# Optimization experiments

Measured on AMD Instinct MI355X. Metric: run time of the kernel, lower is better.

## Reference

```python
import jax, jax.numpy as jnp
import numpy as np

N = 20000
IN_CH = 256
HID = 32
HEADS = 8
OUT_CH = 40
NEG_SLOPE = 0.2


def _gat_layer(x, src, dst, W, a_src, a_dst, b, heads, ch, concat):
    # x: [N, F_in], W: [F_in, heads*ch], a_src/a_dst: [heads, ch], b: [heads*ch] or [ch]
    n = x.shape[0]
    h = (x @ W).reshape(n, heads, ch)                      # [N, H, C]
    alpha_s = jnp.einsum('nhc,hc->nh', h, a_src)           # [N, H]
    alpha_d = jnp.einsum('nhc,hc->nh', h, a_dst)           # [N, H]
    e = jax.nn.leaky_relu(alpha_s[src] + alpha_d[dst], NEG_SLOPE)  # [E, H]
    # segment softmax over edges sharing the same destination node
    m = jax.ops.segment_max(e, dst, num_segments=n)        # [N, H]
    ex = jnp.exp(e - m[dst])                               # [E, H]
    denom = jax.ops.segment_sum(ex, dst, num_segments=n)   # [N, H]
    alpha = ex / (denom[dst] + 1e-16)                      # [E, H]
    out = jax.ops.segment_sum(h[src] * alpha[:, :, None], dst, num_segments=n)  # [N, H, C]
    out = out.reshape(n, heads * ch) if concat else out.mean(axis=1)
    return out + b


def setup_inputs() -> dict:
    key = jax.random.key(0)
    ks = jax.random.split(key, 12)
    x = jax.random.normal(ks[0], (N, IN_CH), dtype=jnp.float32)
    edge_index = jax.random.randint(ks[1], (2, 320000), 0, N, dtype=jnp.int64)
    s1 = 1.0 / np.sqrt(IN_CH)
    s2 = 1.0 / np.sqrt(HEADS * HID)
    W1 = jax.random.uniform(ks[2], (IN_CH, HEADS * HID), jnp.float32, -s1, s1)
    a1_src = jax.random.uniform(ks[3], (HEADS, HID), jnp.float32, -s2, s2)
    a1_dst = jax.random.uniform(ks[4], (HEADS, HID), jnp.float32, -s2, s2)
    b1 = jnp.zeros((HEADS * HID,), jnp.float32)
    W2 = jax.random.uniform(ks[5], (HEADS * HID, OUT_CH), jnp.float32, -s2, s2)
    so = 1.0 / np.sqrt(OUT_CH)
    a2_src = jax.random.uniform(ks[6], (1, OUT_CH), jnp.float32, -so, so)
    a2_dst = jax.random.uniform(ks[7], (1, OUT_CH), jnp.float32, -so, so)
    b2 = jnp.zeros((OUT_CH,), jnp.float32)
    return {"x": x, "edge_index": edge_index, "W1": W1, "a1_src": a1_src,
            "a1_dst": a1_dst, "b1": b1, "W2": W2, "a2_src": a2_src,
            "a2_dst": a2_dst, "b2": b2}


def reference(x, edge_index, W1, a1_src, a1_dst, b1, W2, a2_src, a2_dst, b2):
    n = x.shape[0]
    loop = jnp.arange(n, dtype=edge_index.dtype)
    src = jnp.concatenate([edge_index[0], loop])  # PyG adds self-loops by default
    dst = jnp.concatenate([edge_index[1], loop])
    # dropout layers are identity in eval mode
    h = _gat_layer(x, src, dst, W1, a1_src, a1_dst, b1, HEADS, HID, concat=True)
    h = jax.nn.elu(h)
    out = _gat_layer(h, src, dst, W2, a2_src, a2_dst, b2, 1, OUT_CH, concat=False)
    return jax.nn.log_softmax(out, axis=1)
```

## Files before the change

kernel.cpp:

```cpp
#include <hip/hip_runtime.h>
#include <math.h>

#define N_NODES 20000
#define E_RAW   320000
#define E_TOT   (E_RAW + N_NODES)
#define IN_CH   256
#define HEADS   8
#define HID     32
#define HH      (HEADS*HID)
#define OUT_CH  40
#define NC2     48
#define NEG     0.2f

#define HIST_BLKS ((E_TOT + 255) / 256)
#define G1_BLKS   313

typedef __attribute__((ext_vector_type(8))) short  short8;
typedef __attribute__((ext_vector_type(4))) float  floatx4;

__device__ __forceinline__ unsigned short f2bf(float f) {
    unsigned int u = __float_as_uint(f);
    unsigned int r = (u + 0x7FFFu + ((u >> 16) & 1u)) >> 16;
    return (unsigned short)r;
}
__device__ __forceinline__ float bf2f(unsigned short h) {
    return __uint_as_float(((unsigned int)h) << 16);
}
__device__ __forceinline__ float lexp(float v) {
    v = (v > 0.f) ? v : NEG * v;
    return __expf(v);
}


__global__ void setup_hist(const int* __restrict__ ei,
                           const float* __restrict__ W1,
                           const float* __restrict__ W2,
                           unsigned short* __restrict__ w1t,
                           unsigned short* __restrict__ w2t,
                           int* __restrict__ deg,
                           int* __restrict__ pos) {
    int b = blockIdx.x;
    int t = threadIdx.x;
    if (b < HIST_BLKS) {
        int e = b * 256 + t;
        if (e >= E_TOT) return;
        int d = (e < E_RAW) ? ei[E_RAW + e] : (e - E_RAW);
        pos[e] = atomicAdd(&deg[d], 1);
    } else if (b < HIST_BLKS + HH) {
        int c = b - HIST_BLKS;
        w1t[c * IN_CH + t] = f2bf(W1[(size_t)t * HH + c]);
    } else {
        int c = b - HIST_BLKS - HH;
        w2t[c * HH + t] = (c < OUT_CH) ? f2bf(W2[(size_t)t * OUT_CH + c]) : (unsigned short)0;
    }
}


__global__ __launch_bounds__(1024) void scan_kernel(const int* __restrict__ deg,
                                                    int* __restrict__ offs) {
    __shared__ int wsum[16], wpre[16];
    int t = threadIdx.x;
    int lane = t & 63, wave = t >> 6;
    const int chunk = 20;
    int begin = t * chunk;
    bool in = (begin < N_NODES);
    int loc[20];
    if (in) {
        #pragma unroll
        for (int v4 = 0; v4 < 5; v4++) {
            int4 v = *reinterpret_cast<const int4*>(&deg[begin + v4 * 4]);
            loc[v4*4+0] = v.x; loc[v4*4+1] = v.y; loc[v4*4+2] = v.z; loc[v4*4+3] = v.w;
        }
    } else {
        #pragma unroll
        for (int i = 0; i < 20; i++) loc[i] = 0;
    }
    int s = 0;
    #pragma unroll
    for (int i = 0; i < 20; i++) s += loc[i];
    int sc = s;
    #pragma unroll
    for (int off = 1; off < 64; off <<= 1) {
        int v = __shfl_up(sc, off);
        if (lane >= off) sc += v;
    }
    if (lane == 63) wsum[wave] = sc;
    __syncthreads();
    if (t < 16) {
        int v = wsum[t];
        int p = v;
        #pragma unroll
        for (int off = 1; off < 16; off <<= 1) {
            int u = __shfl_up(p, off);
            if (t >= off) p += u;
        }
        wpre[t] = p - v;
    }
    __syncthreads();
    int run = wpre[wave] + sc - s;
    if (in) {
        #pragma unroll
        for (int v4 = 0; v4 < 5; v4++) {
            int4 o;
            o.x = run; run += loc[v4*4+0];
            o.y = run; run += loc[v4*4+1];
            o.z = run; run += loc[v4*4+2];
            o.w = run; run += loc[v4*4+3];
            *reinterpret_cast<int4*>(&offs[begin + v4 * 4]) = o;
        }
    }
    if (t == 0) offs[N_NODES] = E_TOT;
}

#define G1_LDK 72
__global__ __launch_bounds__(256) void gemm1(const float* __restrict__ x,
                                             const unsigned short* __restrict__ w1t,
                                             const float* __restrict__ a1s,
                                             const float* __restrict__ a1d,
                                             unsigned short* __restrict__ h1b,
                                             float* __restrict__ as1,
                                             float* __restrict__ ad1,
                                             const int* __restrict__ ei,
                                             const int* __restrict__ offs,
                                             const int* __restrict__ pos,
                                             int* __restrict__ csr) {
    __shared__ unsigned short As[64 * G1_LDK];
    __shared__ unsigned short Bs[256 * G1_LDK];
    int t = threadIdx.x;

    if (blockIdx.x >= G1_BLKS) {
        int e = (blockIdx.x - G1_BLKS) * 256 + t;
        if (e < E_TOT) {
            int s, d;
            if (e < E_RAW) { s = ei[e]; d = ei[E_RAW + e]; }
            else           { s = e - E_RAW; d = s; }
            csr[offs[d] + pos[e]] = s;
        }
        return;
    }

    int wave = t >> 6, lane = t & 63;
    int ln = lane & 15, q = lane >> 4;
    int n0 = blockIdx.x * 64;

    floatx4 acc[16];
    #pragma unroll
    for (int f = 0; f < 16; f++) acc[f] = (floatx4){0.f, 0.f, 0.f, 0.f};

    int srow = t >> 4, scol = t & 15;

    for (int kc = 0; kc < IN_CH; kc += 64) {
        #pragma unroll
        for (int pp = 0; pp < 4; pp++) {
            int row = srow + pp * 16;
            int n = n0 + row;
            float4 v = (n < N_NODES)
                ? *reinterpret_cast<const float4*>(&x[(size_t)n * IN_CH + kc + scol * 4])
                : make_float4(0.f, 0.f, 0.f, 0.f);
            ushort4 pv;
            pv.x = f2bf(v.x); pv.y = f2bf(v.y); pv.z = f2bf(v.z); pv.w = f2bf(v.w);
            *reinterpret_cast<ushort4*>(&As[row * G1_LDK + scol * 4]) = pv;
        }
        #pragma unroll
        for (int pp = 0; pp < 16; pp++) {
            int row = srow + pp * 16;
            *reinterpret_cast<ushort4*>(&Bs[row * G1_LDK + scol * 4]) =
                *reinterpret_cast<const ushort4*>(&w1t[(size_t)row * IN_CH + kc + scol * 4]);
        }
        __syncthreads();
        #pragma unroll
        for (int ks = 0; ks < 2; ks++) {
            short8 a = *reinterpret_cast<const short8*>(
                &As[(16 * wave + ln) * G1_LDK + ks * 32 + q * 8]);
            #pragma unroll
            for (int f = 0; f < 16; f++) {
                short8 b = *reinterpret_cast<const short8*>(
                    &Bs[(16 * f + ln) * G1_LDK + ks * 32 + q * 8]);
                acc[f] = __builtin_amdgcn_mfma_f32_16x16x32_bf16(a, b, acc[f], 0, 0, 0);
            }
        }
        __syncthreads();
    }

    float Asr[16], Adr[16];
    #pragma unroll
    for (int f = 0; f < 16; f++) {
        Asr[f] = a1s[16 * f + ln];
        Adr[f] = a1d[16 * f + ln];
    }
    #pragma unroll
    for (int f = 0; f < 16; f++) {
        #pragma unroll
        for (int r = 0; r < 4; r++) {
            int n = n0 + 16 * wave + q * 4 + r;
            if (n < N_NODES)
                h1b[(size_t)n * HH + 16 * f + ln] = f2bf(acc[f][r]);
        }
    }
    #pragma unroll
    for (int lh = 0; lh < 8; lh++) {
        #pragma unroll
        for (int r = 0; r < 4; r++) {
            float ps = acc[2*lh][r] * Asr[2*lh] + acc[2*lh+1][r] * Asr[2*lh+1];
            float pd = acc[2*lh][r] * Adr[2*lh] + acc[2*lh+1][r] * Adr[2*lh+1];
            ps += __shfl_xor(ps, 1); ps += __shfl_xor(ps, 2);
            ps += __shfl_xor(ps, 4); ps += __shfl_xor(ps, 8);
            pd += __shfl_xor(pd, 1); pd += __shfl_xor(pd, 2);
            pd += __shfl_xor(pd, 4); pd += __shfl_xor(pd, 8);
            int n = n0 + 16 * wave + q * 4 + r;
            if (ln == 0 && n < N_NODES) {
                as1[n * HEADS + lh] = ps;
                ad1[n * HEADS + lh] = pd;
            }
        }
    }
}


__global__ __launch_bounds__(256) void aggr1(const unsigned short* __restrict__ h1b,
                                             const float* __restrict__ as1,
                                             const float* __restrict__ ad1,
                                             const float* __restrict__ b1,
                                             const int* __restrict__ offs,
                                             const int* __restrict__ csr,
                                             unsigned short* __restrict__ h2b) {
    int d = blockIdx.x * 4 + (threadIdx.x >> 6);
    int lane = threadIdx.x & 63;
    int h = lane >> 3;
    int c4 = lane * 4;
    int start = offs[d];
    int deg = offs[d + 1] - start;
    float adv = ad1[d * HEADS + h];

    float a0 = 0.f, a1 = 0.f, a2 = 0.f, a3 = 0.f, den = 0.f;
    int jj = 0;
    for (; jj + 8 <= deg; jj += 8) {
        int s[8];
        #pragma unroll
        for (int i = 0; i < 8; i++) s[i] = csr[start + jj + i];
        float e[8];
        #pragma unroll
        for (int i = 0; i < 8; i++) e[i] = as1[s[i] * HEADS + h];
        ushort4 pv[8];
        #pragma unroll
        for (int i = 0; i < 8; i++)
            pv[i] = *reinterpret_cast<const ushort4*>(&h1b[(size_t)s[i] * HH + c4]);
        #pragma unroll
        for (int i = 0; i < 8; i++) {
            float w = lexp(e[i] + adv);
            den += w;
            a0 = fmaf(bf2f(pv[i].x), w, a0);
            a1 = fmaf(bf2f(pv[i].y), w, a1);
            a2 = fmaf(bf2f(pv[i].z), w, a2);
            a3 = fmaf(bf2f(pv[i].w), w, a3);
        }
    }
    for (; jj < deg; jj++) {
        int s = csr[start + jj];
        float w = lexp(as1[s * HEADS + h] + adv);
        den += w;
        ushort4 pv = *reinterpret_cast<const ushort4*>(&h1b[(size_t)s * HH + c4]);
        a0 = fmaf(bf2f(pv.x), w, a0);
        a1 = fmaf(bf2f(pv.y), w, a1);
        a2 = fmaf(bf2f(pv.z), w, a2);
        a3 = fmaf(bf2f(pv.w), w, a3);
    }
    float inv = 1.0f / (den + 1e-16f);
    float4 bv = *reinterpret_cast<const float4*>(&b1[c4]);
    float r0 = a0 * inv + bv.x;
    float r1 = a1 * inv + bv.y;
    float r2 = a2 * inv + bv.z;
    float r3 = a3 * inv + bv.w;
    r0 = (r0 > 0.f) ? r0 : (__expf(r0) - 1.f);
    r1 = (r1 > 0.f) ? r1 : (__expf(r1) - 1.f);
    r2 = (r2 > 0.f) ? r2 : (__expf(r2) - 1.f);
    r3 = (r3 > 0.f) ? r3 : (__expf(r3) - 1.f);
    ushort4 ov;
    ov.x = f2bf(r0); ov.y = f2bf(r1); ov.z = f2bf(r2); ov.w = f2bf(r3);
    *reinterpret_cast<ushort4*>(&h2b[(size_t)d * HH + c4]) = ov;
}

#define G2_LDK 264
__global__ __launch_bounds__(256) void gemm2(const unsigned short* __restrict__ h2b,
                                             const unsigned short* __restrict__ w2t,
                                             const float* __restrict__ a2s,
                                             const float* __restrict__ a2d,
                                             unsigned short* __restrict__ h3b,
                                             float* __restrict__ as2,
                                             float* __restrict__ ad2) {
    __shared__ unsigned short As2[64 * G2_LDK];
    __shared__ unsigned short Bs2[NC2 * G2_LDK];
    int t = threadIdx.x;
    int wave = t >> 6, lane = t & 63;
    int ln = lane & 15, q = lane >> 4;
    int n0 = blockIdx.x * 64;

    {
        int row = t >> 2, seg = t & 3;
        int n = n0 + row;
        #pragma unroll
        for (int i = 0; i < 8; i++) {
            short8 v;
            if (n < N_NODES)
                v = *reinterpret_cast<const short8*>(&h2b[(size_t)n * HH + seg * 64 + i * 8]);
            else
                v = (short8){0,0,0,0,0,0,0,0};
            *reinterpret_cast<short8*>(&As2[row * G2_LDK + seg * 64 + i * 8]) = v;
        }
    }
    for (int u = t; u < NC2 * 32; u += 256) {
        int row = u >> 5;
        int col = (u & 31) * 8;
        *reinterpret_cast<short8*>(&Bs2[row * G2_LDK + col]) =
            *reinterpret_cast<const short8*>(&w2t[(size_t)row * HH + col]);
    }
    __syncthreads();

    floatx4 acc[3];
    #pragma unroll
    for (int f = 0; f < 3; f++) acc[f] = (floatx4){0.f, 0.f, 0.f, 0.f};

    #pragma unroll
    for (int kf = 0; kf < 8; kf++) {
        short8 a = *reinterpret_cast<const short8*>(
            &As2[(16 * wave + ln) * G2_LDK + kf * 32 + q * 8]);
        #pragma unroll
        for (int f = 0; f < 3; f++) {
            short8 b = *reinterpret_cast<const short8*>(
                &Bs2[(16 * f + ln) * G2_LDK + kf * 32 + q * 8]);
            acc[f] = __builtin_amdgcn_mfma_f32_16x16x32_bf16(a, b, acc[f], 0, 0, 0);
        }
    }

    float a2sv[3], a2dv[3];
    #pragma unroll
    for (int f = 0; f < 3; f++) {
        int c = 16 * f + ln;
        a2sv[f] = (c < OUT_CH) ? a2s[c] : 0.f;
        a2dv[f] = (c < OUT_CH) ? a2d[c] : 0.f;
    }
    #pragma unroll
    for (int r = 0; r < 4; r++) {
        int n = n0 + 16 * wave + q * 4 + r;
        float ps = acc[0][r] * a2sv[0] + acc[1][r] * a2sv[1] + acc[2][r] * a2sv[2];
        float pd = acc[0][r] * a2dv[0] + acc[1][r] * a2dv[1] + acc[2][r] * a2dv[2];
        ps += __shfl_xor(ps, 1); ps += __shfl_xor(ps, 2);
        ps += __shfl_xor(ps, 4); ps += __shfl_xor(ps, 8);
        pd += __shfl_xor(pd, 1); pd += __shfl_xor(pd, 2);
        pd += __shfl_xor(pd, 4); pd += __shfl_xor(pd, 8);
        if (n < N_NODES) {
            #pragma unroll
            for (int f = 0; f < 3; f++) {
                int c = 16 * f + ln;
                if (c < OUT_CH)
                    h3b[(size_t)n * OUT_CH + c] = f2bf(acc[f][r]);
            }
            if (ln == 0) { as2[n] = ps; ad2[n] = pd; }
        }
    }
}


__global__ __launch_bounds__(256) void aggr2(const unsigned short* __restrict__ h3b,
                                             const float* __restrict__ as2,
                                             const float* __restrict__ ad2,
                                             const float* __restrict__ b2,
                                             const int* __restrict__ offs,
                                             const int* __restrict__ csr,
                                             float* __restrict__ out) {
    int d = blockIdx.x * 4 + (threadIdx.x >> 6);
    int lane = threadIdx.x & 63;
    int start = offs[d];
    int deg = offs[d + 1] - start;
    float adv = ad2[d];
    bool ok = (lane < OUT_CH);
    int cl = ok ? lane : 0;

    float acc = 0.f, den = 0.f;
    int jj = 0;
    for (; jj + 8 <= deg; jj += 8) {
        int s[8];
        #pragma unroll
        for (int i = 0; i < 8; i++) s[i] = csr[start + jj + i];
        float e[8];
        #pragma unroll
        for (int i = 0; i < 8; i++) e[i] = as2[s[i]];
        unsigned short qv[8];
        #pragma unroll
        for (int i = 0; i < 8; i++) qv[i] = h3b[(size_t)s[i] * OUT_CH + cl];
        #pragma unroll
        for (int i = 0; i < 8; i++) {
            float w = lexp(e[i] + adv);
            den += w;
            acc = fmaf(bf2f(qv[i]), w, acc);
        }
    }
    for (; jj < deg; jj++) {
        int s = csr[start + jj];
        float w = lexp(as2[s] + adv);
        den += w;
        acc = fmaf(bf2f(h3b[(size_t)s * OUT_CH + cl]), w, acc);
    }

    float r = ok ? (acc / (den + 1e-16f) + b2[lane]) : -1e30f;
    float mx = r;
    #pragma unroll
    for (int off = 32; off >= 1; off >>= 1) mx = fmaxf(mx, __shfl_xor(mx, off));
    float ex = ok ? __expf(r - mx) : 0.f;
    float se = ex;
    #pragma unroll
    for (int off = 32; off >= 1; off >>= 1) se += __shfl_xor(se, off);
    if (ok) out[(size_t)d * OUT_CH + lane] = r - mx - __logf(se);
}


extern "C" void kernel_launch(void* const* d_in, const int* in_sizes, int n_in,
                              void* d_out, int out_size, void* d_ws, size_t ws_size,
                              hipStream_t stream) {
    const float* x   = (const float*)d_in[0];
    const int*   ei  = (const int*)  d_in[1];
    const float* W1  = (const float*)d_in[2];
    const float* a1s = (const float*)d_in[3];
    const float* a1d = (const float*)d_in[4];
    const float* b1  = (const float*)d_in[5];
    const float* W2  = (const float*)d_in[6];
    const float* a2s = (const float*)d_in[7];
    const float* a2d = (const float*)d_in[8];
    const float* b2  = (const float*)d_in[9];
    float* out = (float*)d_out;

    char* p = (char*)d_ws;
    auto alloc = [&](size_t bytes) {
        char* r = p;
        p += (bytes + 255) & ~(size_t)255;
        return r;
    };
    unsigned short* h1b = (unsigned short*)alloc((size_t)N_NODES * HH * 2);
    unsigned short* h2b = (unsigned short*)alloc((size_t)N_NODES * HH * 2);
    unsigned short* h3b = (unsigned short*)alloc((size_t)N_NODES * OUT_CH * 2);
    unsigned short* w1t = (unsigned short*)alloc((size_t)IN_CH * HH * 2);
    unsigned short* w2t = (unsigned short*)alloc((size_t)NC2 * HH * 2);
    float* as1  = (float*)alloc((size_t)N_NODES * HEADS * 4);
    float* ad1  = (float*)alloc((size_t)N_NODES * HEADS * 4);
    float* as2v = (float*)alloc((size_t)N_NODES * 4);
    float* ad2v = (float*)alloc((size_t)N_NODES * 4);
    int* deg    = (int*)alloc((size_t)N_NODES * 4);
    int* pos    = (int*)alloc((size_t)E_TOT * 4);
    int* offs   = (int*)alloc((size_t)(N_NODES + 1) * 4);
    int* csr    = (int*)alloc((size_t)E_TOT * 4);

    hipMemsetAsync(deg, 0, (size_t)N_NODES * sizeof(int), stream);
    setup_hist<<<HIST_BLKS + HH + NC2, 256, 0, stream>>>(ei, W1, W2, w1t, w2t, deg, pos);
    scan_kernel<<<1, 1024, 0, stream>>>(deg, offs);
    gemm1<<<G1_BLKS + HIST_BLKS, 256, 0, stream>>>(x, w1t, a1s, a1d, h1b, as1, ad1,
                                                   ei, offs, pos, csr);
    aggr1<<<N_NODES / 4, 256, 0, stream>>>(h1b, as1, ad1, b1, offs, csr, h2b);
    gemm2<<<313, 256, 0, stream>>>(h2b, w2t, a2s, a2d, h3b, as2v, ad2v);
    aggr2<<<N_NODES / 4, 256, 0, stream>>>(h3b, as2v, ad2v, b2, offs, csr, out);
}
```

Measured before the change: 192.7 us.

## Pre-convert x to bf16 and stage GEMM tiles via direct global-to-LDS loads

x is converted to bf16 once in the setup kernel. Both GEMMs now fill shared memory with global_load_lds 16-byte direct copies into XOR-swizzled tiles, replacing register-staged padded loads. gemm1 keeps the whole 64x256 A tile resident and streams B in K chunks. This is meant to cut VGPR staging and LDS bank conflicts, but it adds an extra bf16 copy of x in the workspace, extra setup blocks, and unguarded reads past N_NODES that depend on padded buffers. The padding rows are never initialized, though they only feed output rows that are discarded.

```diff
diff --git a/kernel.cpp b/kernel.cpp
--- a/kernel.cpp
+++ b/kernel.cpp
@@ -2,6 +2,7 @@
 #include <math.h>
 
 #define N_NODES 20000
+#define N_PAD   20032
 #define E_RAW   320000
 #define E_TOT   (E_RAW + N_NODES)
 #define IN_CH   256
@@ -13,6 +14,7 @@
 #define NEG     0.2f
 
 #define HIST_BLKS ((E_TOT + 255) / 256)
+#define XB_BLKS   (N_NODES / 8)
 #define G1_BLKS   313
 
 typedef __attribute__((ext_vector_type(8))) short  short8;
@@ -31,12 +33,20 @@
     return __expf(v);
 }
 
+__device__ __forceinline__ void gload16(const void* g, void* l) {
+    __builtin_amdgcn_global_load_lds(
+        (const __attribute__((address_space(1))) void*)g,
+        (__attribute__((address_space(3))) void*)l, 16, 0, 0);
+}
+
 
 __global__ void setup_hist(const int* __restrict__ ei,
+                           const float* __restrict__ x,
                            const float* __restrict__ W1,
                            const float* __restrict__ W2,
                            unsigned short* __restrict__ w1t,
                            unsigned short* __restrict__ w2t,
+                           unsigned short* __restrict__ xb,
                            int* __restrict__ deg,
                            int* __restrict__ pos) {
     int b = blockIdx.x;
@@ -49,9 +59,21 @@
     } else if (b < HIST_BLKS + HH) {
         int c = b - HIST_BLKS;
         w1t[c * IN_CH + t] = f2bf(W1[(size_t)t * HH + c]);
-    } else {
+    } else if (b < HIST_BLKS + HH + NC2) {
         int c = b - HIST_BLKS - HH;
         w2t[c * HH + t] = (c < OUT_CH) ? f2bf(W2[(size_t)t * OUT_CH + c]) : (unsigned short)0;
+    } else {
+        int bb = b - (HIST_BLKS + HH + NC2);
+        int n = bb * 8 + (t >> 5);
+        int c0 = (t & 31) * 8;
+        const float4* src = reinterpret_cast<const float4*>(&x[(size_t)n * IN_CH + c0]);
+        float4 v0 = src[0], v1 = src[1];
+        short8 sv;
+        sv[0] = (short)f2bf(v0.x); sv[1] = (short)f2bf(v0.y);
+        sv[2] = (short)f2bf(v0.z); sv[3] = (short)f2bf(v0.w);
+        sv[4] = (short)f2bf(v1.x); sv[5] = (short)f2bf(v1.y);
+        sv[6] = (short)f2bf(v1.z); sv[7] = (short)f2bf(v1.w);
+        *reinterpret_cast<short8*>(&xb[(size_t)n * IN_CH + c0]) = sv;
     }
 }
 
@@ -112,8 +134,8 @@
     if (t == 0) offs[N_NODES] = E_TOT;
 }
 
-#define G1_LDK 72
-__global__ __launch_bounds__(256) void gemm1(const float* __restrict__ x,
+
+__global__ __launch_bounds__(256) void gemm1(const unsigned short* __restrict__ xb,
                                              const unsigned short* __restrict__ w1t,
                                              const float* __restrict__ a1s,
                                              const float* __restrict__ a1d,
@@ -124,8 +146,8 @@
                                              const int* __restrict__ offs,
                                              const int* __restrict__ pos,
                                              int* __restrict__ csr) {
-    __shared__ unsigned short As[64 * G1_LDK];
-    __shared__ unsigned short Bs[256 * G1_LDK];
+    __shared__ unsigned char Al[64 * 512];
+    __shared__ unsigned char Bl[256 * 128];
     int t = threadIdx.x;
 
     if (blockIdx.x >= G1_BLKS) {
@@ -142,44 +164,57 @@
     int wave = t >> 6, lane = t & 63;
     int ln = lane & 15, q = lane >> 4;
     int n0 = blockIdx.x * 64;
+    const char* xbase = (const char*)xb + (size_t)n0 * 512;
+    const char* bbase = (const char*)w1t;
+
+    #pragma unroll
+    for (int j = 0; j < 8; j++) {
+        int R = (wave * 8 + j) * 1024;
+        int o = R + lane * 16;
+        int r = o >> 9;
+        int cb = (o & 511) ^ ((r & 7) << 4);
+        gload16(xbase + (size_t)r * 512 + cb, &Al[R]);
+    }
+    #pragma unroll
+    for (int j = 0; j < 8; j++) {
+        int R = (wave * 8 + j) * 1024;
+        int o = R + lane * 16;
+        int r = o >> 7;
+        int cb = (o & 127) ^ ((r & 7) << 4);
+        gload16(bbase + (size_t)r * 512 + cb, &Bl[R]);
+    }
+    __syncthreads();
 
     floatx4 acc[16];
     #pragma unroll
     for (int f = 0; f < 16; f++) acc[f] = (floatx4){0.f, 0.f, 0.f, 0.f};
 
-    int srow = t >> 4, scol = t & 15;
-
-    for (int kc = 0; kc < IN_CH; kc += 64) {
-        #pragma unroll
-        for (int pp = 0; pp < 4; pp++) {
-            int row = srow + pp * 16;
-            int n = n0 + row;
-            float4 v = (n < N_NODES)
-                ? *reinterpret_cast<const float4*>(&x[(size_t)n * IN_CH + kc + scol * 4])
-                : make_float4(0.f, 0.f, 0.f, 0.f);
-            ushort4 pv;
-            pv.x = f2bf(v.x); pv.y = f2bf(v.y); pv.z = f2bf(v.z); pv.w = f2bf(v.w);
-            *reinterpret_cast<ushort4*>(&As[row * G1_LDK + scol * 4]) = pv;
-        }
-        #pragma unroll
-        for (int pp = 0; pp < 16; pp++) {
-            int row = srow + pp * 16;
-            *reinterpret_cast<ushort4*>(&Bs[row * G1_LDK + scol * 4]) =
-                *reinterpret_cast<const ushort4*>(&w1t[(size_t)row * IN_CH + kc + scol * 4]);
-        }
-        __syncthreads();
+    int xorv = (ln & 7) << 4;
+
+    for (int c = 0; c < 4; c++) {
         #pragma unroll
         for (int ks = 0; ks < 2; ks++) {
-            short8 a = *reinterpret_cast<const short8*>(
-                &As[(16 * wave + ln) * G1_LDK + ks * 32 + q * 8]);
+            int ao = (16 * wave + ln) * 512 + c * 128 + ((ks * 64 + q * 16) ^ xorv);
+            short8 a = *reinterpret_cast<const short8*>(&Al[ao]);
+            int bo0 = ln * 128 + ((ks * 64 + q * 16) ^ xorv);
             #pragma unroll
             for (int f = 0; f < 16; f++) {
-                short8 b = *reinterpret_cast<const short8*>(
-                    &Bs[(16 * f + ln) * G1_LDK + ks * 32 + q * 8]);
-                acc[f] = __builtin_amdgcn_mfma_f32_16x16x32_bf16(a, b, acc[f], 0, 0, 0);
+                short8 bfr = *reinterpret_cast<const short8*>(&Bl[bo0 + f * 2048]);
+                acc[f] = __builtin_amdgcn_mfma_f32_16x16x32_bf16(a, bfr, acc[f], 0, 0, 0);
             }
         }
-        __syncthreads();
+        if (c < 3) {
+            __syncthreads();
+            #pragma unroll
+            for (int j = 0; j < 8; j++) {
+                int R = (wave * 8 + j) * 1024;
+                int o = R + lane * 16;
+                int r = o >> 7;
+                int cb = (o & 127) ^ ((r & 7) << 4);
+                gload16(bbase + (size_t)r * 512 + (c + 1) * 128 + cb, &Bl[R]);
+            }
+            __syncthreads();
+        }
     }
 
     float Asr[16], Adr[16];
@@ -280,7 +315,7 @@
     *reinterpret_cast<ushort4*>(&h2b[(size_t)d * HH + c4]) = ov;
 }
 
-#define G2_LDK 264
+
 __global__ __launch_bounds__(256) void gemm2(const unsigned short* __restrict__ h2b,
                                              const unsigned short* __restrict__ w2t,
                                              const float* __restrict__ a2s,
@@ -288,31 +323,30 @@
                                              unsigned short* __restrict__ h3b,
                                              float* __restrict__ as2,
                                              float* __restrict__ ad2) {
-    __shared__ unsigned short As2[64 * G2_LDK];
-    __shared__ unsigned short Bs2[NC2 * G2_LDK];
+    __shared__ unsigned char Al[64 * 512];
+    __shared__ unsigned char Bl[NC2 * 512];
     int t = threadIdx.x;
     int wave = t >> 6, lane = t & 63;
     int ln = lane & 15, q = lane >> 4;
     int n0 = blockIdx.x * 64;
-
-    {
-        int row = t >> 2, seg = t & 3;
-        int n = n0 + row;
-        #pragma unroll
-        for (int i = 0; i < 8; i++) {
-            short8 v;
-            if (n < N_NODES)
-                v = *reinterpret_cast<const short8*>(&h2b[(size_t)n * HH + seg * 64 + i * 8]);
-            else
-                v = (short8){0,0,0,0,0,0,0,0};
-            *reinterpret_cast<short8*>(&As2[row * G2_LDK + seg * 64 + i * 8]) = v;
-        }
-    }
-    for (int u = t; u < NC2 * 32; u += 256) {
-        int row = u >> 5;
-        int col = (u & 31) * 8;
-        *reinterpret_cast<short8*>(&Bs2[row * G2_LDK + col]) =
-            *reinterpret_cast<const short8*>(&w2t[(size_t)row * HH + col]);
+    const char* abase = (const char*)h2b + (size_t)n0 * 512;
+    const char* bbase = (const char*)w2t;
+
+    #pragma unroll
+    for (int j = 0; j < 8; j++) {
+        int R = (wave * 8 + j) * 1024;
+        int o = R + lane * 16;
+        int r = o >> 9;
+        int cb = (o & 511) ^ ((r & 7) << 4);
+        gload16(abase + (size_t)r * 512 + cb, &Al[R]);
+    }
+    #pragma unroll
+    for (int j = 0; j < 6; j++) {
+        int R = (wave * 6 + j) * 1024;
+        int o = R + lane * 16;
+        int r = o >> 9;
+        int cb = (o & 511) ^ ((r & 7) << 4);
+        gload16(bbase + (size_t)r * 512 + cb, &Bl[R]);
     }
     __syncthreads();
 
@@ -320,15 +354,17 @@
     #pragma unroll
     for (int f = 0; f < 3; f++) acc[f] = (floatx4){0.f, 0.f, 0.f, 0.f};
 
+    int xorv = (ln & 7) << 4;
+
     #pragma unroll
     for (int kf = 0; kf < 8; kf++) {
-        short8 a = *reinterpret_cast<const short8*>(
-            &As2[(16 * wave + ln) * G2_LDK + kf * 32 + q * 8]);
+        int ao = ((16 * wave + ln) * 512 + kf * 64 + q * 16) ^ xorv;
+        short8 a = *reinterpret_cast<const short8*>(&Al[ao]);
+        int bo0 = (ln * 512 + kf * 64 + q * 16) ^ xorv;
         #pragma unroll
         for (int f = 0; f < 3; f++) {
-            short8 b = *reinterpret_cast<const short8*>(
-                &Bs2[(16 * f + ln) * G2_LDK + kf * 32 + q * 8]);
-            acc[f] = __builtin_amdgcn_mfma_f32_16x16x32_bf16(a, b, acc[f], 0, 0, 0);
+            short8 bfr = *reinterpret_cast<const short8*>(&Bl[bo0 + f * 8192]);
+            acc[f] = __builtin_amdgcn_mfma_f32_16x16x32_bf16(a, bfr, acc[f], 0, 0, 0);
         }
     }
 
@@ -435,8 +471,9 @@
         p += (bytes + 255) & ~(size_t)255;
         return r;
     };
+    unsigned short* xb  = (unsigned short*)alloc((size_t)N_PAD * IN_CH * 2);
     unsigned short* h1b = (unsigned short*)alloc((size_t)N_NODES * HH * 2);
-    unsigned short* h2b = (unsigned short*)alloc((size_t)N_NODES * HH * 2);
+    unsigned short* h2b = (unsigned short*)alloc((size_t)N_PAD * HH * 2);
     unsigned short* h3b = (unsigned short*)alloc((size_t)N_NODES * OUT_CH * 2);
     unsigned short* w1t = (unsigned short*)alloc((size_t)IN_CH * HH * 2);
     unsigned short* w2t = (unsigned short*)alloc((size_t)NC2 * HH * 2);
@@ -450,9 +487,10 @@
     int* csr    = (int*)alloc((size_t)E_TOT * 4);
 
     hipMemsetAsync(deg, 0, (size_t)N_NODES * sizeof(int), stream);
-    setup_hist<<<HIST_BLKS + HH + NC2, 256, 0, stream>>>(ei, W1, W2, w1t, w2t, deg, pos);
+    setup_hist<<<HIST_BLKS + HH + NC2 + XB_BLKS, 256, 0, stream>>>(
+        ei, x, W1, W2, w1t, w2t, xb, deg, pos);
     scan_kernel<<<1, 1024, 0, stream>>>(deg, offs);
-    gemm1<<<G1_BLKS + HIST_BLKS, 256, 0, stream>>>(x, w1t, a1s, a1d, h1b, as1, ad1,
+    gemm1<<<G1_BLKS + HIST_BLKS, 256, 0, stream>>>(xb, w1t, a1s, a1d, h1b, as1, ad1,
                                                    ei, offs, pos, csr);
     aggr1<<<N_NODES / 4, 256, 0, stream>>>(h1b, as1, ad1, b1, offs, csr, h2b);
     gemm2<<<313, 256, 0, stream>>>(h2b, w2t, a2s, a2d, h3b, as2v, ad2v);
```

Result: faster. 172.9 us (-10.2%).
